# Kernel optimization log

Hardware: AMD Instinct MI355X
Metric: run time of the kernel (lower is better)

The kernel has to match this reference:

```python
import jax, jax.numpy as jnp
import numpy as np

B, D, N, TS = 8, 256, 12306, 4
OUT = TS ** 3 * 3  # 192


def setup_inputs() -> dict:
    key = jax.random.key(0)
    ks = jax.random.split(key, 9)

    def w(k, shape, fan_in):
        return jax.random.normal(k, shape, dtype=jnp.float32) * (1.0 / np.sqrt(fan_in))

    return {
        "latent_x": jax.random.normal(ks[0], (B, 1, D), dtype=jnp.float32),
        "W1": w(ks[1], (512, D), D), "b1": jnp.zeros((512,), jnp.float32),
        "W2": w(ks[2], (1024, 512), 512), "b2": jnp.zeros((1024,), jnp.float32),
        "W3": w(ks[3], (512, 1024), 1024), "b3": jnp.zeros((512,), jnp.float32),
        "W4": w(ks[4], (OUT, 512), 512), "b4": jnp.zeros((OUT,), jnp.float32),
    }


def reference(latent_x, W1, b1, W2, b2, W3, b3, W4, b4):
    # latent_x: (B, 1, D). The torch code repeats it num_points times along dim 1
    # and runs kernel-size-1 convs, so every point produces the identical value;
    # we evaluate the MLP once per batch element (same math, no redundancy).
    z = latent_x[:, 0, :]                      # (B, D)
    g = lambda t: jax.nn.gelu(t, approximate=False)  # nn.GELU() default = exact erf
    h = g(z @ W1.T + b1)                       # (B, 512)
    h = g(h @ W2.T + b2)                       # (B, 1024)
    h = g(h @ W3.T + b3)                       # (B, 512)
    o = jax.nn.sigmoid(h @ W4.T + b4)          # (B, 192)
    # Faithful to torch: conv output is (B, 192, N) contiguous, then .view
    # reinterprets row-major into (B, N, ts, ts, ts, 3) WITHOUT a transpose.
    full = jnp.broadcast_to(o[:, :, None], (B, OUT, N))  # (B, 192, N)
    return full.reshape(B, N, TS, TS, TS, 3)
```

## Files before the change

kernel.cpp:

```cpp
#include <hip/hip_runtime.h>
#include <hip/hip_bf16.h>
#include <cstdint>

#define BATCH 8
#define NREP 12306
#define OUTC 192

__device__ __forceinline__ float gelu_exact(float x) {
    return 0.5f * x * (1.0f + erff(x * 0.70710678118654752f));
}
__device__ __forceinline__ float sigmoidf_(float x) {
    return 1.0f / (1.0f + __expf(-x));
}

template <int K, int R, int ACT>
__global__ __launch_bounds__(256) void gemv_layer(const float* __restrict__ in,
                                                  const float* __restrict__ W,
                                                  const float* __restrict__ bias,
                                                  float* __restrict__ out) {
    __shared__ float s_in[BATCH * K];
    for (int i = threadIdx.x; i < BATCH * K; i += 256) s_in[i] = in[i];
    __syncthreads();

    const int wave = threadIdx.x >> 6;
    const int lane = threadIdx.x & 63;
    const int row  = blockIdx.x * 4 + wave;
    if (row >= R) return;

    constexpr int NV = K / 256;
    float4 wv[NV];
    const float4* Wrow = reinterpret_cast<const float4*>(W + (size_t)row * K);
#pragma unroll
    for (int i = 0; i < NV; ++i) wv[i] = Wrow[i * 64 + lane];

    float acc[BATCH];
#pragma unroll
    for (int b = 0; b < BATCH; ++b) {
        const float4* sb = reinterpret_cast<const float4*>(s_in + b * K);
        float a = 0.0f;
#pragma unroll
        for (int i = 0; i < NV; ++i) {
            const float4 iv = sb[i * 64 + lane];
            a += wv[i].x * iv.x + wv[i].y * iv.y + wv[i].z * iv.z + wv[i].w * iv.w;
        }
        acc[b] = a;
    }

#pragma unroll
    for (int b = 0; b < BATCH; ++b) {
#pragma unroll
        for (int s = 32; s > 0; s >>= 1) acc[b] += __shfl_xor(acc[b], s, 64);
    }

    if (lane == 0) {
        const float bb = bias[row];
#pragma unroll
        for (int b = 0; b < BATCH; ++b) {
            float x = acc[b] + bb;
            out[b * R + row] = (ACT == 0) ? gelu_exact(x) : sigmoidf_(x);
        }
    }
}

__global__ __launch_bounds__(256) void broadcast_kernel(const float* __restrict__ o,
                                                        float* __restrict__ out) {
    const int bp = blockIdx.x;
    const float v = o[bp];
    const size_t e0 = (size_t)bp * NREP;
    float* p = out + e0;
    const int t = threadIdx.x;

    const int mis  = (int)(e0 & 3);
    const int head = mis ? (4 - mis) : 0;
    if (t < head) p[t] = v;

    const int n_main4 = (NREP - head) >> 2;
    float4 vv = make_float4(v, v, v, v);
    float4* p4 = reinterpret_cast<float4*>(p + head);
    for (int j = t; j < n_main4; j += 256) p4[j] = vv;

    const int done = head + (n_main4 << 2);
    const int tail = NREP - done;
    if (t < tail) p[done + t] = v;
}

extern "C" void kernel_launch(void* const* d_in, const int* in_sizes, int n_in,
                              void* d_out, int out_size, void* d_ws, size_t ws_size,
                              hipStream_t stream) {
    const float* latent = (const float*)d_in[0];
    const float* W1 = (const float*)d_in[1];
    const float* b1 = (const float*)d_in[2];
    const float* W2 = (const float*)d_in[3];
    const float* b2 = (const float*)d_in[4];
    const float* W3 = (const float*)d_in[5];
    const float* b3 = (const float*)d_in[6];
    const float* W4 = (const float*)d_in[7];
    const float* b4 = (const float*)d_in[8];
    float* out = (float*)d_out;

    float* ws = (float*)d_ws;
    float* h1 = ws;
    float* h2 = h1 + BATCH * 512;
    float* h3 = h2 + BATCH * 1024;
    float* o  = h3 + BATCH * 512;

    gemv_layer< 256,  512, 0><<<512 / 4,  256, 0, stream>>>(latent, W1, b1, h1);
    gemv_layer< 512, 1024, 0><<<1024 / 4, 256, 0, stream>>>(h1,     W2, b2, h2);
    gemv_layer<1024,  512, 0><<<512 / 4,  256, 0, stream>>>(h2,     W3, b3, h3);
    gemv_layer< 512,  192, 1><<<192 / 4,  256, 0, stream>>>(h3,     W4, b4, o);

    broadcast_kernel<<<BATCH * OUTC, 256, 0, stream>>>(o, out);
}
```

Before: 123.3 us.

## Fuse MLP layers and broadcast into one persistent kernel with grid barriers

Replaces the four GEMV launches and the broadcast launch with a single 256-block kernel. Between layers it synchronizes through atomic-counter grid barriers, and the counters are reset by a memset each call. Inputs are now read directly from global memory instead of being staged in shared memory. This removes per-launch overhead and inter-kernel gaps, but it depends on all 256 blocks being co-resident, and the spin barriers plus the extra memset add their own latency.

```diff
diff --git a/kernel.cpp b/kernel.cpp
--- a/kernel.cpp
+++ b/kernel.cpp
@@ -5,6 +5,9 @@
 #define BATCH 8
 #define NREP 12306
 #define OUTC 192
+#define NBLOCKS 256
+#define NTHREADS 256
+#define RUNS_PER_BLOCK ((BATCH * OUTC) / NBLOCKS)
 
 __device__ __forceinline__ float gelu_exact(float x) {
     return 0.5f * x * (1.0f + erff(x * 0.70710678118654752f));
@@ -13,20 +16,26 @@
     return 1.0f / (1.0f + __expf(-x));
 }
 
+__device__ __forceinline__ void grid_barrier(unsigned int* ctr) {
+    __syncthreads();
+    if (threadIdx.x == 0) {
+        __threadfence();
+        __hip_atomic_fetch_add(ctr, 1u, __ATOMIC_RELEASE, __HIP_MEMORY_SCOPE_AGENT);
+        while (__hip_atomic_load(ctr, __ATOMIC_ACQUIRE, __HIP_MEMORY_SCOPE_AGENT)
+               < (unsigned int)NBLOCKS) {
+            __builtin_amdgcn_s_sleep(1);
+        }
+        __threadfence();
+    }
+    __syncthreads();
+}
+
 template <int K, int R, int ACT>
-__global__ __launch_bounds__(256) void gemv_layer(const float* __restrict__ in,
-                                                  const float* __restrict__ W,
-                                                  const float* __restrict__ bias,
-                                                  float* __restrict__ out) {
-    __shared__ float s_in[BATCH * K];
-    for (int i = threadIdx.x; i < BATCH * K; i += 256) s_in[i] = in[i];
-    __syncthreads();
-
-    const int wave = threadIdx.x >> 6;
+__device__ __forceinline__ void gemv_body(const float* __restrict__ in,
+                                          const float* __restrict__ W,
+                                          const float* __restrict__ bias,
+                                          float* __restrict__ out, int row) {
     const int lane = threadIdx.x & 63;
-    const int row  = blockIdx.x * 4 + wave;
-    if (row >= R) return;
-
     constexpr int NV = K / 256;
     float4 wv[NV];
     const float4* Wrow = reinterpret_cast<const float4*>(W + (size_t)row * K);
@@ -36,52 +45,71 @@
     float acc[BATCH];
 #pragma unroll
     for (int b = 0; b < BATCH; ++b) {
-        const float4* sb = reinterpret_cast<const float4*>(s_in + b * K);
+        const float4* ib = reinterpret_cast<const float4*>(in + b * K);
         float a = 0.0f;
 #pragma unroll
         for (int i = 0; i < NV; ++i) {
-            const float4 iv = sb[i * 64 + lane];
-            a += wv[i].x * iv.x + wv[i].y * iv.y + wv[i].z * iv.z + wv[i].w * iv.w;
+            const float4 iv = ib[i * 64 + lane];
+            a = fmaf(wv[i].x, iv.x, a);
+            a = fmaf(wv[i].y, iv.y, a);
+            a = fmaf(wv[i].z, iv.z, a);
+            a = fmaf(wv[i].w, iv.w, a);
         }
         acc[b] = a;
     }
-
 #pragma unroll
     for (int b = 0; b < BATCH; ++b) {
 #pragma unroll
         for (int s = 32; s > 0; s >>= 1) acc[b] += __shfl_xor(acc[b], s, 64);
     }
-
     if (lane == 0) {
         const float bb = bias[row];
 #pragma unroll
         for (int b = 0; b < BATCH; ++b) {
-            float x = acc[b] + bb;
+            const float x = acc[b] + bb;
             out[b * R + row] = (ACT == 0) ? gelu_exact(x) : sigmoidf_(x);
         }
     }
 }
 
-__global__ __launch_bounds__(256) void broadcast_kernel(const float* __restrict__ o,
-                                                        float* __restrict__ out) {
-    const int bp = blockIdx.x;
-    const float v = o[bp];
-    const size_t e0 = (size_t)bp * NREP;
-    float* p = out + e0;
+__global__ __launch_bounds__(NTHREADS) void fused_decoder(
+        const float* __restrict__ latent,
+        const float* __restrict__ W1, const float* __restrict__ b1,
+        const float* __restrict__ W2, const float* __restrict__ b2,
+        const float* __restrict__ W3, const float* __restrict__ b3,
+        const float* __restrict__ W4, const float* __restrict__ b4,
+        float* __restrict__ h1, float* __restrict__ h2,
+        float* __restrict__ h3, float* __restrict__ o,
+        unsigned int* __restrict__ ctrs,
+        float* __restrict__ out) {
+    const int gw = blockIdx.x * (NTHREADS / 64) + (threadIdx.x >> 6);
+
+    if (gw < 512)  gemv_body< 256,  512, 0>(latent, W1, b1, h1, gw);
+    grid_barrier(ctrs + 0);
+    if (gw < 1024) gemv_body< 512, 1024, 0>(h1, W2, b2, h2, gw);
+    grid_barrier(ctrs + 1);
+    if (gw < 512)  gemv_body<1024,  512, 0>(h2, W3, b3, h3, gw);
+    grid_barrier(ctrs + 2);
+    if (gw < OUTC) gemv_body< 512, OUTC, 1>(h3, W4, b4, o, gw);
+    grid_barrier(ctrs + 3);
+
     const int t = threadIdx.x;
-
-    const int mis  = (int)(e0 & 3);
-    const int head = mis ? (4 - mis) : 0;
-    if (t < head) p[t] = v;
-
-    const int n_main4 = (NREP - head) >> 2;
-    float4 vv = make_float4(v, v, v, v);
-    float4* p4 = reinterpret_cast<float4*>(p + head);
-    for (int j = t; j < n_main4; j += 256) p4[j] = vv;
-
-    const int done = head + (n_main4 << 2);
-    const int tail = NREP - done;
-    if (t < tail) p[done + t] = v;
+#pragma unroll
+    for (int j = 0; j < RUNS_PER_BLOCK; ++j) {
+        const int bp = blockIdx.x * RUNS_PER_BLOCK + j;
+        const float v = o[bp];
+        const size_t e0 = (size_t)bp * NREP;
+        float* p = out + e0;
+        const int mis  = (int)(e0 & 3);
+        const int head = mis ? (4 - mis) : 0;
+        if (t < head) p[t] = v;
+        const int n4 = (NREP - head) >> 2;
+        const float4 vv = make_float4(v, v, v, v);
+        float4* p4 = reinterpret_cast<float4*>(p + head);
+        for (int i = t; i < n4; i += NTHREADS) p4[i] = vv;
+        const int done = head + (n4 << 2);
+        if (t < NREP - done) p[done + t] = v;
+    }
 }
 
 extern "C" void kernel_launch(void* const* d_in, const int* in_sizes, int n_in,
@@ -103,11 +131,9 @@
     float* h2 = h1 + BATCH * 512;
     float* h3 = h2 + BATCH * 1024;
     float* o  = h3 + BATCH * 512;
+    unsigned int* ctrs = (unsigned int*)((char*)d_ws + 80 * 1024);
 
-    gemv_layer< 256,  512, 0><<<512 / 4,  256, 0, stream>>>(latent, W1, b1, h1);
-    gemv_layer< 512, 1024, 0><<<1024 / 4, 256, 0, stream>>>(h1,     W2, b2, h2);
-    gemv_layer<1024,  512, 0><<<512 / 4,  256, 0, stream>>>(h2,     W3, b3, h3);
-    gemv_layer< 512,  192, 1><<<192 / 4,  256, 0, stream>>>(h3,     W4, b4, o);
-
-    broadcast_kernel<<<BATCH * OUTC, 256, 0, stream>>>(o, out);
+    hipMemsetAsync(ctrs, 0, 64, stream);
+    fused_decoder<<<NBLOCKS, NTHREADS, 0, stream>>>(
+        latent, W1, b1, W2, b2, W3, b3, W4, b4, h1, h2, h3, o, ctrs, out);
 }
```

New measurement: 205.1 us. 66.4% more time.
